# Kernel optimization log

Hardware: AMD Instinct MI355X
Metric: run time of the kernel (lower is better)

Reference implementation:

```python
import jax, jax.numpy as jnp
import numpy as np

L = 4        # n_layers
C = 512      # channels = d_model
NH = 16      # n_heads
DH = 32      # d_head (hard-coded in source)
DFF = 4 * C  # FeedForward hidden size
B, HH, WW = 4, 32, 32
GN_GROUPS, GN_EPS, LN_EPS = 16, 1e-6, 1e-5


def setup_inputs() -> dict:
    key = jax.random.key(0)
    ks = jax.random.split(key, 32)
    w = lambda k, s: (jax.random.normal(k, s, jnp.float32) * 0.02)
    return {
        "x": jax.random.normal(ks[0], (B, C, HH, WW), jnp.float32),
        # GroupNorm affine
        "gn_w": jnp.ones((C,), jnp.float32),
        "gn_b": jnp.zeros((C,), jnp.float32),
        # 1x1 conv in/out, stored as [C_in, C_out]
        "pin_w": w(ks[1], (C, C)), "pin_b": jnp.zeros((C,), jnp.float32),
        "pout_w": w(ks[2], (C, C)), "pout_b": jnp.zeros((C,), jnp.float32),
        # per-layer stacked params
        "ln1_w": jnp.ones((L, C), jnp.float32), "ln1_b": jnp.zeros((L, C), jnp.float32),
        "wq": w(ks[3], (L, C, C)), "wk": w(ks[4], (L, C, C)), "wv": w(ks[5], (L, C, C)),
        "wo": w(ks[6], (L, C, C)), "bo": jnp.zeros((L, C), jnp.float32),
        "ln3_w": jnp.ones((L, C), jnp.float32), "ln3_b": jnp.zeros((L, C), jnp.float32),
        "ff1_w": w(ks[7], (L, C, 2 * DFF)), "ff1_b": jnp.zeros((L, 2 * DFF), jnp.float32),
        "ff2_w": w(ks[8], (L, DFF, C)), "ff2_b": jnp.zeros((L, C), jnp.float32),
    }


def _group_norm(x, w, b):
    bsz, c, h, ww = x.shape
    xg = x.reshape(bsz, GN_GROUPS, c // GN_GROUPS, h, ww)
    m = xg.mean(axis=(2, 3, 4), keepdims=True)
    v = xg.var(axis=(2, 3, 4), keepdims=True)
    xn = ((xg - m) * jax.lax.rsqrt(v + GN_EPS)).reshape(bsz, c, h, ww)
    return xn * w[None, :, None, None] + b[None, :, None, None]


def _layer_norm(x, w, b):
    m = x.mean(axis=-1, keepdims=True)
    v = x.var(axis=-1, keepdims=True)
    return (x - m) * jax.lax.rsqrt(v + LN_EPS) * w + b


def reference(x, gn_w, gn_b, pin_w, pin_b, pout_w, pout_b,
              ln1_w, ln1_b, wq, wk, wv, wo, bo,
              ln3_w, ln3_b, ff1_w, ff1_b, ff2_w, ff2_b):
    b, c, h, w_ = x.shape
    x_in = x
    x = _group_norm(x, gn_w, gn_b)
    x = jnp.einsum('bchw,co->bohw', x, pin_w) + pin_b[None, :, None, None]
    x = x.transpose(0, 2, 3, 1).reshape(b, h * w_, c)  # [b, n, c]
    n = h * w_
    nh = c // DH
    scale = DH ** -0.5
    for l in range(L):
        hx = _layer_norm(x, ln1_w[l], ln1_b[l])
        q = (hx @ wq[l]).reshape(b, n, nh, DH)
        k = (hx @ wk[l]).reshape(b, n, nh, DH)
        v = (hx @ wv[l]).reshape(b, n, nh, DH)
        attn = jax.nn.softmax(jnp.einsum('bihd,bjhd->bhij', q, k) * scale, axis=-1)
        o = jnp.einsum('bhij,bjhd->bihd', attn, v).reshape(b, n, c)
        x = o @ wo[l] + bo[l] + x
        hx = _layer_norm(x, ln3_w[l], ln3_b[l])
        p = hx @ ff1_w[l] + ff1_b[l]
        a, g = jnp.split(p, 2, axis=-1)
        x = (a * jax.nn.gelu(g, approximate=False)) @ ff2_w[l] + ff2_b[l] + x
    x = x.reshape(b, h, w_, c).transpose(0, 3, 1, 2)
    x = jnp.einsum('bchw,co->bohw', x, pout_w) + pout_b[None, :, None, None]
    return x + x_in
```

## Files before the change

### kernel.cpp

```cpp
#include <hip/hip_runtime.h>
#include <math.h>


typedef __bf16 bf16x8_t __attribute__((ext_vector_type(8)));
typedef float f32x4 __attribute__((ext_vector_type(4)));

__device__ __forceinline__ unsigned short f2bf(float f) {
  unsigned u = __float_as_uint(f);
  return (unsigned short)((u + 0x7FFFu + ((u >> 16) & 1u)) >> 16);
}
__device__ __forceinline__ float gelu_exact(float x) {
  return 0.5f * x * (1.f + erff(x * 0.70710678118654752440f));
}

__global__ __launch_bounds__(256) void gn_kernel(
    const float* __restrict__ X, const float* __restrict__ w,
    const float* __restrict__ b, float* __restrict__ Y) {
  int blk = blockIdx.x;
  int g = blk & 15;
  const float* xp = X + (size_t)blk * 32 * 1024;
  float* yp = Y + (size_t)blk * 32 * 1024;
  int tid = threadIdx.x;
  float sum = 0.f, sq = 0.f;
  const float4* x4 = (const float4*)xp;
  for (int i = tid; i < 8192; i += 256) {
    float4 v = x4[i];
    sum += v.x + v.y + v.z + v.w;
    sq += v.x * v.x + v.y * v.y + v.z * v.z + v.w * v.w;
  }
  #pragma unroll
  for (int off = 32; off; off >>= 1) {
    sum += __shfl_xor(sum, off);
    sq += __shfl_xor(sq, off);
  }
  __shared__ float s0[4], s1[4];
  int wid = tid >> 6, lane = tid & 63;
  if (lane == 0) { s0[wid] = sum; s1[wid] = sq; }
  __syncthreads();
  sum = s0[0] + s0[1] + s0[2] + s0[3];
  sq = s1[0] + s1[1] + s1[2] + s1[3];
  float mean = sum * (1.f / 32768.f);
  float var = sq * (1.f / 32768.f) - mean * mean;
  float rstd = rsqrtf(var + 1e-6f);
  float4* y4 = (float4*)yp;
  for (int i = tid; i < 8192; i += 256) {
    int ch = g * 32 + (i >> 8);
    float sc = rstd * w[ch];
    float sh = b[ch] - mean * sc;
    float4 v = x4[i];
    float4 o;
    o.x = v.x * sc + sh; o.y = v.y * sc + sh;
    o.z = v.z * sc + sh; o.w = v.w * sc + sh;
    y4[i] = o;
  }
}

__global__ __launch_bounds__(256) void ln_kernel(
    const float* __restrict__ X, const float* __restrict__ w,
    const float* __restrict__ b, unsigned short* __restrict__ Y) {
  int row = blockIdx.x * 4 + (threadIdx.x >> 6);
  int lane = threadIdx.x & 63;
  const float4* xr = (const float4*)(X + (size_t)row * 512);
  float4 v0 = xr[lane];
  float4 v1 = xr[lane + 64];
  float sum = v0.x + v0.y + v0.z + v0.w + v1.x + v1.y + v1.z + v1.w;
  float sq = v0.x * v0.x + v0.y * v0.y + v0.z * v0.z + v0.w * v0.w +
             v1.x * v1.x + v1.y * v1.y + v1.z * v1.z + v1.w * v1.w;
  #pragma unroll
  for (int off = 32; off; off >>= 1) {
    sum += __shfl_xor(sum, off);
    sq += __shfl_xor(sq, off);
  }
  float mean = sum * (1.f / 512.f);
  float var = sq * (1.f / 512.f) - mean * mean;
  float rstd = rsqrtf(var + 1e-5f);
  unsigned short* yr = Y + (size_t)row * 512;
  int c0 = lane * 4, c1 = lane * 4 + 256;
  const float4 w0 = *(const float4*)&w[c0], b0v = *(const float4*)&b[c0];
  const float4 w1 = *(const float4*)&w[c1], b1v = *(const float4*)&b[c1];
  unsigned p0 = (unsigned)f2bf((v0.x - mean) * rstd * w0.x + b0v.x) |
                ((unsigned)f2bf((v0.y - mean) * rstd * w0.y + b0v.y) << 16);
  unsigned p1 = (unsigned)f2bf((v0.z - mean) * rstd * w0.z + b0v.z) |
                ((unsigned)f2bf((v0.w - mean) * rstd * w0.w + b0v.w) << 16);
  unsigned p2 = (unsigned)f2bf((v1.x - mean) * rstd * w1.x + b1v.x) |
                ((unsigned)f2bf((v1.y - mean) * rstd * w1.y + b1v.y) << 16);
  unsigned p3 = (unsigned)f2bf((v1.z - mean) * rstd * w1.z + b1v.z) |
                ((unsigned)f2bf((v1.w - mean) * rstd * w1.w + b1v.w) << 16);
  uint2 q0 = {p0, p1}, q1 = {p2, p3};
  *(uint2*)&yr[c0] = q0;
  *(uint2*)&yr[c1] = q1;
}

__global__ void wtc_kernel(const float* __restrict__ in,
                           unsigned short* __restrict__ out, int rows,
                           int cols, float scale) {
  __shared__ float t[32][33];
  int z = blockIdx.z;
  const float* ip = in + (size_t)z * rows * cols;
  unsigned short* op = out + (size_t)z * rows * cols;
  int r0 = blockIdx.y * 32, c0 = blockIdx.x * 32;
  for (int rr = threadIdx.y; rr < 32; rr += 8)
    t[rr][threadIdx.x] = ip[(size_t)(r0 + rr) * cols + c0 + threadIdx.x];
  __syncthreads();
  for (int rr = threadIdx.y; rr < 32; rr += 8)
    op[(size_t)(c0 + rr) * rows + r0 + threadIdx.x] =
        f2bf(t[threadIdx.x][rr] * scale);
}

template <int TM, int TN, int MODE>
__global__ __launch_bounds__(256) void mgemm(
    const short* __restrict__ A, int lda, const short* __restrict__ B0,
    const short* __restrict__ B1, const short* __restrict__ B2, float* C0,
    float* C1, float* C2, unsigned short* Cb, int ldc,
    const float* __restrict__ bias, const float* resid, int K, int ggoff) {
  constexpr int WM = TM / 2, WN = TN / 2, MF = WM / 16, NF = WN / 16;
  constexpr int ASL = TM / 32;
  constexpr int BSL = TN / 32;
  __shared__ short As[2][TM][64];
  __shared__ short Bs[2][TN][64];
  __shared__ short Bs2[MODE == 2 ? 2 : 1][MODE == 2 ? TN : 1][64];

  const short* B = B0;
  float* C = C0;
  if (blockIdx.z == 1) { B = B1; C = C1; }
  else if (blockIdx.z == 2) { B = B2; C = C2; }
  const short* Bg = (MODE == 2) ? B0 + (size_t)ggoff * K : nullptr;

  int tid = threadIdx.x;
  int bm = blockIdx.y * TM, bn = blockIdx.x * TN;

  f32x4 acc[MF][NF];
  f32x4 acc2[MODE == 2 ? MF : 1][MODE == 2 ? NF : 1];
  #pragma unroll
  for (int m = 0; m < MF; ++m)
    #pragma unroll
    for (int n = 0; n < NF; ++n) {
      acc[m][n] = (f32x4)0.f;
      if (MODE == 2) acc2[m][n] = (f32x4)0.f;
    }

  int wid = tid >> 6, lane = tid & 63;
  int wr = wid >> 1, wc = wid & 1;
  int lrow = lane & 15, lhk = lane >> 4;

  bf16x8_t ra[ASL], rb[BSL], rb2[MODE == 2 ? BSL : 1];

  auto load_regs = [&](int k0) {
    #pragma unroll
    for (int i = 0; i < ASL; ++i) {
      int slot = tid + i * 256, r = slot >> 3, s = slot & 7;
      ra[i] = *(const bf16x8_t*)(A + (size_t)(bm + r) * lda + k0 + s * 8);
    }
    #pragma unroll
    for (int i = 0; i < BSL; ++i) {
      int slot = tid + i * 256, r = slot >> 3, s = slot & 7;
      rb[i] = *(const bf16x8_t*)(B + (size_t)(bn + r) * K + k0 + s * 8);
      if (MODE == 2)
        rb2[i] = *(const bf16x8_t*)(Bg + (size_t)(bn + r) * K + k0 + s * 8);
    }
  };
  auto store_lds = [&](int bufi) {
    #pragma unroll
    for (int i = 0; i < ASL; ++i) {
      int slot = tid + i * 256, r = slot >> 3, s = slot & 7;
      *(bf16x8_t*)&As[bufi][r][(s ^ (r & 7)) * 8] = ra[i];
    }
    #pragma unroll
    for (int i = 0; i < BSL; ++i) {
      int slot = tid + i * 256, r = slot >> 3, s = slot & 7;
      *(bf16x8_t*)&Bs[bufi][r][(s ^ (r & 7)) * 8] = rb[i];
      if (MODE == 2) *(bf16x8_t*)&Bs2[bufi][r][(s ^ (r & 7)) * 8] = rb2[i];
    }
  };
  auto compute = [&](int bufi) {
    bf16x8_t af[2][MF], bfr[2][NF], bf2[MODE == 2 ? 2 : 1][MODE == 2 ? NF : 1];
    #pragma unroll
    for (int ks = 0; ks < 2; ++ks) {
      int sl = ks * 4 + lhk;
      int ph = (sl ^ (lrow & 7)) * 8;
      #pragma unroll
      for (int m = 0; m < MF; ++m)
        af[ks][m] = *(const bf16x8_t*)&As[bufi][wr * WM + m * 16 + lrow][ph];
      #pragma unroll
      for (int n = 0; n < NF; ++n) {
        bfr[ks][n] = *(const bf16x8_t*)&Bs[bufi][wc * WN + n * 16 + lrow][ph];
        if (MODE == 2)
          bf2[ks][n] = *(const bf16x8_t*)&Bs2[bufi][wc * WN + n * 16 + lrow][ph];
      }
    }
    #pragma unroll
    for (int ks = 0; ks < 2; ++ks)
      #pragma unroll
      for (int m = 0; m < MF; ++m)
        #pragma unroll
        for (int n = 0; n < NF; ++n) {
          acc[m][n] = __builtin_amdgcn_mfma_f32_16x16x32_bf16(
              af[ks][m], bfr[ks][n], acc[m][n], 0, 0, 0);
          if (MODE == 2)
            acc2[m][n] = __builtin_amdgcn_mfma_f32_16x16x32_bf16(
                af[ks][m], bf2[ks][n], acc2[m][n], 0, 0, 0);
        }
  };

  int ns = K >> 6;
  load_regs(0);
  store_lds(0);
  __syncthreads();
  int buf = 0;
  for (int t = 0; t < ns; ++t) {
    bool more = (t + 1 < ns);
    if (more) load_regs((t + 1) << 6);
    compute(buf);
    if (more) store_lds(buf ^ 1);
    __syncthreads();
    buf ^= 1;
  }

  int row0 = bm + wr * WM + lhk * 4;
  int col0 = bn + wc * WN + lrow;
  #pragma unroll
  for (int m = 0; m < MF; ++m) {
    #pragma unroll
    for (int n = 0; n < NF; ++n) {
      int col = col0 + n * 16;
      if (MODE == 0) {
        float bv = bias ? bias[col] : 0.f;
        #pragma unroll
        for (int j = 0; j < 4; ++j) {
          int row = row0 + m * 16 + j;
          C[(size_t)row * ldc + col] = acc[m][n][j] + bv;
        }
      } else if (MODE == 1) {
        float bv = bias[col];
        #pragma unroll
        for (int j = 0; j < 4; ++j) {
          int row = row0 + m * 16 + j;
          float v = acc[m][n][j] + bv + resid[(size_t)row * ldc + col];
          C[(size_t)row * ldc + col] = v;
          Cb[(size_t)row * ldc + col] = f2bf(v);
        }
      } else if (MODE == 2) {
        float ba = bias[col], bg = bias[ggoff + col];
        #pragma unroll
        for (int j = 0; j < 4; ++j) {
          int row = row0 + m * 16 + j;
          float a = acc[m][n][j] + ba;
          float g = acc2[m][n][j] + bg;
          Cb[(size_t)row * ldc + col] = f2bf(a * gelu_exact(g));
        }
      } else {
        unsigned short* Co = (unsigned short*)C;
        #pragma unroll
        for (int j = 0; j < 4; ++j) {
          int row = row0 + m * 16 + j;
          Co[(size_t)row * ldc + col] = f2bf(acc[m][n][j]);
        }
      }
    }
  }
}

__global__ __launch_bounds__(256) void fattn_kernel(
    const unsigned short* __restrict__ Q, const unsigned short* __restrict__ K,
    const unsigned short* __restrict__ V, unsigned short* __restrict__ O) {
  constexpr int QT = 128, KT = 64;
  __shared__ __bf16 Ks[KT][40];
  __shared__ __bf16 Vs[32][68];
  __shared__ __bf16 Ps[4][32][68];

  int h = blockIdx.y, bb = blockIdx.z;
  int q0 = blockIdx.x * QT;
  int tid = threadIdx.x;
  int wid = tid >> 6, lane = tid & 63;
  int lrow = lane & 15, lhk = lane >> 4;

  const unsigned short* Qb = Q + (size_t)bb * 1024 * 512 + h * 32;
  const unsigned short* Kb = K + (size_t)bb * 1024 * 512 + h * 32;
  const unsigned short* Vb = V + (size_t)bb * 1024 * 512 + h * 32;

  bf16x8_t qa[2];
  #pragma unroll
  for (int m = 0; m < 2; ++m)
    qa[m] = *(const bf16x8_t*)(
        Qb + (size_t)(q0 + wid * 32 + m * 16 + lrow) * 512 + lhk * 8);

  int kr = tid >> 2, kp = tid & 3;
  int vk = tid & 63, vd0 = (tid >> 6) * 8;

  bf16x8_t kreg, vreg;
  auto gload = [&](int kt) {
    kreg = *(const bf16x8_t*)(Kb + (size_t)(kt + kr) * 512 + kp * 8);
    vreg = *(const bf16x8_t*)(Vb + (size_t)(kt + vk) * 512 + vd0);
  };
  auto sstore = [&]() {
    *(bf16x8_t*)&Ks[kr][kp * 8] = kreg;
    #pragma unroll
    for (int i = 0; i < 8; ++i) Vs[vd0 + i][vk] = vreg[i];
  };

  f32x4 o[2][2];
  float lpart[2][4];
  #pragma unroll
  for (int m = 0; m < 2; ++m) {
    o[m][0] = (f32x4)0.f; o[m][1] = (f32x4)0.f;
    #pragma unroll
    for (int j = 0; j < 4; ++j) lpart[m][j] = 0.f;
  }

  gload(0);
  for (int t = 0; t < 16; ++t) {
    sstore();
    __syncthreads();
    if (t < 15) gload((t + 1) * KT);

    bf16x8_t kb[4];
    #pragma unroll
    for (int n = 0; n < 4; ++n)
      kb[n] = *(const bf16x8_t*)&Ks[n * 16 + lrow][lhk * 8];
    f32x4 s[2][4];
    #pragma unroll
    for (int m = 0; m < 2; ++m)
      #pragma unroll
      for (int n = 0; n < 4; ++n)
        s[m][n] = __builtin_amdgcn_mfma_f32_16x16x32_bf16(qa[m], kb[n],
                                                          (f32x4)0.f, 0, 0, 0);

    #pragma unroll
    for (int m = 0; m < 2; ++m)
      #pragma unroll
      for (int j = 0; j < 4; ++j) {
        float p0 = __expf(s[m][0][j]), p1 = __expf(s[m][1][j]);
        float p2 = __expf(s[m][2][j]), p3 = __expf(s[m][3][j]);
        lpart[m][j] += (p0 + p1) + (p2 + p3);
        int prow = m * 16 + lhk * 4 + j;
        Ps[wid][prow][lrow] = (__bf16)p0;
        Ps[wid][prow][16 + lrow] = (__bf16)p1;
        Ps[wid][prow][32 + lrow] = (__bf16)p2;
        Ps[wid][prow][48 + lrow] = (__bf16)p3;
      }

    #pragma unroll
    for (int ks = 0; ks < 2; ++ks) {
      bf16x8_t pa[2], vbf[2];
      #pragma unroll
      for (int m = 0; m < 2; ++m)
        pa[m] = *(const bf16x8_t*)&Ps[wid][m * 16 + lrow][ks * 32 + lhk * 8];
      #pragma unroll
      for (int dn = 0; dn < 2; ++dn)
        vbf[dn] = *(const bf16x8_t*)&Vs[dn * 16 + lrow][ks * 32 + lhk * 8];
      #pragma unroll
      for (int m = 0; m < 2; ++m)
        #pragma unroll
        for (int dn = 0; dn < 2; ++dn)
          o[m][dn] = __builtin_amdgcn_mfma_f32_16x16x32_bf16(pa[m], vbf[dn],
                                                             o[m][dn], 0, 0, 0);
    }
    __syncthreads();
  }

  #pragma unroll
  for (int m = 0; m < 2; ++m)
    #pragma unroll
    for (int j = 0; j < 4; ++j) {
      float l = lpart[m][j];
      #pragma unroll
      for (int off = 1; off < 16; off <<= 1) l += __shfl_xor(l, off);
      float inv = 1.f / l;
      int row = q0 + wid * 32 + m * 16 + lhk * 4 + j;
      #pragma unroll
      for (int dn = 0; dn < 2; ++dn)
        O[(size_t)(bb * 1024 + row) * 512 + h * 32 + dn * 16 + lrow] =
            __builtin_bit_cast(unsigned short, (__bf16)(o[m][dn][j] * inv));
    }
}

__global__ void out_kernel(const float* __restrict__ y,
                           const float* __restrict__ pb,
                           const float* __restrict__ xin,
                           float* __restrict__ out) {
  __shared__ float t[32][33];
  int b = blockIdx.z;
  int o0 = blockIdx.x * 32, n0 = blockIdx.y * 32;
  const float* yp = y + (size_t)b * 1024 * 512;
  for (int rr = threadIdx.y; rr < 32; rr += 8)
    t[rr][threadIdx.x] = yp[(size_t)(n0 + rr) * 512 + o0 + threadIdx.x];
  __syncthreads();
  for (int rr = threadIdx.y; rr < 32; rr += 8) {
    int o = o0 + rr;
    size_t idx = ((size_t)b * 512 + o) * 1024 + n0 + threadIdx.x;
    out[idx] = t[threadIdx.x][rr] + pb[o] + xin[idx];
  }
}

extern "C" void kernel_launch(void* const* d_in, const int* in_sizes, int n_in,
                              void* d_out, int out_size, void* d_ws,
                              size_t ws_size, hipStream_t stream) {
  const float* x_in = (const float*)d_in[0];
  const float* gn_w = (const float*)d_in[1];
  const float* gn_b = (const float*)d_in[2];
  const float* pin_w = (const float*)d_in[3];
  const float* pin_b = (const float*)d_in[4];
  const float* pout_w = (const float*)d_in[5];
  const float* pout_b = (const float*)d_in[6];
  const float* ln1_w = (const float*)d_in[7];
  const float* ln1_b = (const float*)d_in[8];
  const float* wq = (const float*)d_in[9];
  const float* wk = (const float*)d_in[10];
  const float* wv = (const float*)d_in[11];
  const float* wo = (const float*)d_in[12];
  const float* bo = (const float*)d_in[13];
  const float* ln3_w = (const float*)d_in[14];
  const float* ln3_b = (const float*)d_in[15];
  const float* ff1_w = (const float*)d_in[16];
  const float* ff1_b = (const float*)d_in[17];
  const float* ff2_w = (const float*)d_in[18];
  const float* ff2_b = (const float*)d_in[19];

  char* wsb = (char*)d_ws;
  float* XTOK = (float*)wsb;
  char* R = wsb + (8u << 20);
  unsigned short* Qbf = (unsigned short*)R;
  unsigned short* Kbf = (unsigned short*)(R + (4u << 20));
  unsigned short* Vbf = (unsigned short*)(R + (8u << 20));
  unsigned short* G2b = (unsigned short*)R;
  float* XTy = (float*)(R + (16u << 20));
  float* GNt = (float*)R;
  unsigned short* XTb = (unsigned short*)(wsb + (32u << 20));
  unsigned short* HXb = (unsigned short*)(wsb + (36u << 20));
  unsigned short* Obf = (unsigned short*)(wsb + (40u << 20));
  unsigned short* XTOKb = (unsigned short*)(wsb + (44u << 20));
  unsigned short* W = (unsigned short*)(wsb + (48u << 20));
  const size_t S = 262144;
  unsigned short* pinT = W;
  unsigned short* poutT = W + S;
  unsigned short* wqT = W + 2 * S;
  unsigned short* wkT = wqT + 4 * S;
  unsigned short* wvT = wkT + 4 * S;
  unsigned short* woT = wvT + 4 * S;
  unsigned short* ff1T = woT + 4 * S;
  unsigned short* ff2T = ff1T + 4 * (512 * 4096);

  dim3 tb32(32, 8);
  const float qscale = 0.17677669529663687f;

  wtc_kernel<<<dim3(16, 16, 1), tb32, 0, stream>>>(pin_w, pinT, 512, 512, 1.f);
  wtc_kernel<<<dim3(16, 16, 1), tb32, 0, stream>>>(pout_w, poutT, 512, 512, 1.f);
  wtc_kernel<<<dim3(16, 16, 4), tb32, 0, stream>>>(wq, wqT, 512, 512, qscale);
  wtc_kernel<<<dim3(16, 16, 4), tb32, 0, stream>>>(wk, wkT, 512, 512, 1.f);
  wtc_kernel<<<dim3(16, 16, 4), tb32, 0, stream>>>(wv, wvT, 512, 512, 1.f);
  wtc_kernel<<<dim3(16, 16, 4), tb32, 0, stream>>>(wo, woT, 512, 512, 1.f);
  wtc_kernel<<<dim3(128, 16, 4), tb32, 0, stream>>>(ff1_w, ff1T, 512, 4096, 1.f);
  wtc_kernel<<<dim3(16, 64, 4), tb32, 0, stream>>>(ff2_w, ff2T, 2048, 512, 1.f);

  gn_kernel<<<64, 256, 0, stream>>>(x_in, gn_w, gn_b, GNt);
  wtc_kernel<<<dim3(32, 16, 4), tb32, 0, stream>>>(GNt, XTb, 512, 1024, 1.f);
  mgemm<128, 64, 0><<<dim3(8, 32, 1), 256, 0, stream>>>(
      (const short*)XTb, 512, (const short*)pinT, nullptr, nullptr, XTOK,
      nullptr, nullptr, nullptr, 512, pin_b, nullptr, 512, 0);

  for (int l = 0; l < 4; ++l) {
    const short* wqT_l = (const short*)(wqT + (size_t)l * S);
    const short* wkT_l = (const short*)(wkT + (size_t)l * S);
    const short* wvT_l = (const short*)(wvT + (size_t)l * S);
    const short* woT_l = (const short*)(woT + (size_t)l * S);
    const short* ff1T_l = (const short*)(ff1T + (size_t)l * 512 * 4096);
    const short* ff2T_l = (const short*)(ff2T + (size_t)l * 2048 * 512);

    ln_kernel<<<1024, 256, 0, stream>>>(XTOK, ln1_w + l * 512, ln1_b + l * 512,
                                        HXb);
    mgemm<128, 64, 3><<<dim3(8, 32, 3), 256, 0, stream>>>(
        (const short*)HXb, 512, wqT_l, wkT_l, wvT_l, (float*)Qbf, (float*)Kbf,
        (float*)Vbf, nullptr, 512, nullptr, nullptr, 512, 0);
    fattn_kernel<<<dim3(8, 16, 4), 256, 0, stream>>>(Qbf, Kbf, Vbf, Obf);
    mgemm<128, 64, 1><<<dim3(8, 32, 1), 256, 0, stream>>>(
        (const short*)Obf, 512, woT_l, nullptr, nullptr, XTOK, nullptr,
        nullptr, XTOKb, 512, bo + l * 512, XTOK, 512, 0);
    ln_kernel<<<1024, 256, 0, stream>>>(XTOK, ln3_w + l * 512, ln3_b + l * 512,
                                        HXb);
    mgemm<128, 64, 2><<<dim3(32, 32, 1), 256, 0, stream>>>(
        (const short*)HXb, 512, ff1T_l, nullptr, nullptr, nullptr, nullptr,
        nullptr, G2b, 2048, ff1_b + l * 4096, nullptr, 512, 2048);
    mgemm<128, 64, 1><<<dim3(8, 32, 1), 256, 0, stream>>>(
        (const short*)G2b, 2048, ff2T_l, nullptr, nullptr, XTOK, nullptr,
        nullptr, XTOKb, 512, ff2_b + l * 512, XTOK, 2048, 0);
  }
  mgemm<128, 64, 0><<<dim3(8, 32, 1), 256, 0, stream>>>(
      (const short*)XTOKb, 512, (const short*)poutT, nullptr, nullptr, XTy,
      nullptr, nullptr, nullptr, 512, nullptr, nullptr, 512, 0);
  out_kernel<<<dim3(16, 32, 4), tb32, 0, stream>>>(XTy, pout_b, x_in,
                                                   (float*)d_out);
}
```

Baseline: 580.1 us.

## Batch weight conversions into one launch, fuse GN apply and output epilogue, XCD-aware tile mapping

Replaces the nine separate weight transpose/convert launches with one table-driven conversion kernel. The GroupNorm apply step moves into the input transpose through per-channel scale/shift values, so the normalized fp32 intermediate is never written out. The final out-projection GEMM gets a new epilogue that writes NCHW output with bias and residual directly, which removes out_kernel and its scratch buffer. GEMM block indices are remapped so that each XCD takes a contiguous band of M rows for better L2 locality, at the cost of extra index arithmetic.

```diff
diff --git a/kernel.cpp b/kernel.cpp
--- a/kernel.cpp
+++ b/kernel.cpp
@@ -13,16 +13,15 @@
   return 0.5f * x * (1.f + erff(x * 0.70710678118654752440f));
 }
 
-__global__ __launch_bounds__(256) void gn_kernel(
+__global__ __launch_bounds__(256) void gn_stats(
     const float* __restrict__ X, const float* __restrict__ w,
-    const float* __restrict__ b, float* __restrict__ Y) {
+    const float* __restrict__ b, float* __restrict__ sc,
+    float* __restrict__ sh) {
   int blk = blockIdx.x;
-  int g = blk & 15;
-  const float* xp = X + (size_t)blk * 32 * 1024;
-  float* yp = Y + (size_t)blk * 32 * 1024;
+  int g = blk & 15, bb = blk >> 4;
+  const float4* x4 = (const float4*)(X + (size_t)blk * 32768);
   int tid = threadIdx.x;
   float sum = 0.f, sq = 0.f;
-  const float4* x4 = (const float4*)xp;
   for (int i = tid; i < 8192; i += 256) {
     float4 v = x4[i];
     sum += v.x + v.y + v.z + v.w;
@@ -42,17 +41,47 @@
   float mean = sum * (1.f / 32768.f);
   float var = sq * (1.f / 32768.f) - mean * mean;
   float rstd = rsqrtf(var + 1e-6f);
-  float4* y4 = (float4*)yp;
-  for (int i = tid; i < 8192; i += 256) {
-    int ch = g * 32 + (i >> 8);
-    float sc = rstd * w[ch];
-    float sh = b[ch] - mean * sc;
-    float4 v = x4[i];
-    float4 o;
-    o.x = v.x * sc + sh; o.y = v.y * sc + sh;
-    o.z = v.z * sc + sh; o.w = v.w * sc + sh;
-    y4[i] = o;
-  }
+  if (tid < 32) {
+    int ch = g * 32 + tid;
+    float s_ = rstd * w[ch];
+    sc[bb * 512 + ch] = s_;
+    sh[bb * 512 + ch] = b[ch] - mean * s_;
+  }
+}
+
+struct CvtEnt {
+  const float* src; unsigned short* dst;
+  const float* rs; const float* rsh;
+  int rows, cols, nmat, pre; float scale;
+};
+struct CvtTab { CvtEnt e[9]; };
+
+__global__ __launch_bounds__(256) void cvt_all(CvtTab tab) {
+  __shared__ float t[32][33];
+  int blk = blockIdx.x;
+  int ei = 0;
+  #pragma unroll
+  for (int i = 1; i < 9; ++i)
+    if (blk >= tab.e[i].pre) ei = i;
+  const CvtEnt E = tab.e[ei];
+  int local = blk - E.pre;
+  int tcx = E.cols >> 5;
+  int tpm = tcx * (E.rows >> 5);
+  int mat = local / tpm, tt = local - mat * tpm;
+  int r0 = (tt / tcx) << 5, c0 = (tt - (tt / tcx) * tcx) << 5;
+  const float* sp = E.src + (size_t)mat * E.rows * E.cols;
+  unsigned short* dp = E.dst + (size_t)mat * E.rows * E.cols;
+  const float* rsp = E.rs ? E.rs + (size_t)mat * E.rows : nullptr;
+  const float* rshp = E.rsh ? E.rsh + (size_t)mat * E.rows : nullptr;
+  int tx = threadIdx.x;
+  for (int rr = threadIdx.y; rr < 32; rr += 8) {
+    float s_ = rsp ? rsp[r0 + rr] : E.scale;
+    float h_ = rshp ? rshp[r0 + rr] : 0.f;
+    t[rr][tx] = sp[(size_t)(r0 + rr) * E.cols + c0 + tx] * s_ + h_;
+  }
+  __syncthreads();
+  for (int rr = threadIdx.y; rr < 32; rr += 8)
+    dp[(size_t)(c0 + rr) * E.rows + r0 + tx] = f2bf(t[tx][rr]);
 }
 
 __global__ __launch_bounds__(256) void ln_kernel(
@@ -91,22 +120,6 @@
   *(uint2*)&yr[c1] = q1;
 }
 
-__global__ void wtc_kernel(const float* __restrict__ in,
-                           unsigned short* __restrict__ out, int rows,
-                           int cols, float scale) {
-  __shared__ float t[32][33];
-  int z = blockIdx.z;
-  const float* ip = in + (size_t)z * rows * cols;
-  unsigned short* op = out + (size_t)z * rows * cols;
-  int r0 = blockIdx.y * 32, c0 = blockIdx.x * 32;
-  for (int rr = threadIdx.y; rr < 32; rr += 8)
-    t[rr][threadIdx.x] = ip[(size_t)(r0 + rr) * cols + c0 + threadIdx.x];
-  __syncthreads();
-  for (int rr = threadIdx.y; rr < 32; rr += 8)
-    op[(size_t)(c0 + rr) * rows + r0 + threadIdx.x] =
-        f2bf(t[threadIdx.x][rr] * scale);
-}
-
 template <int TM, int TN, int MODE>
 __global__ __launch_bounds__(256) void mgemm(
     const short* __restrict__ A, int lda, const short* __restrict__ B0,
@@ -120,14 +133,25 @@
   __shared__ short Bs[2][TN][64];
   __shared__ short Bs2[MODE == 2 ? 2 : 1][MODE == 2 ? TN : 1][64];
 
+  int flat = (blockIdx.z * gridDim.y + blockIdx.y) * gridDim.x + blockIdx.x;
+  int xcd = flat & 7;
+  int pos = flat >> 3;
+  int gz = gridDim.z;
+  int zz = pos % gz;
+  pos /= gz;
+  int bandH = gridDim.y >> 3;
+  int m_loc = pos % bandH;
+  int bn_i = pos / bandH;
+  int bm = (xcd * bandH + m_loc) * TM;
+  int bn = bn_i * TN;
+
   const short* B = B0;
   float* C = C0;
-  if (blockIdx.z == 1) { B = B1; C = C1; }
-  else if (blockIdx.z == 2) { B = B2; C = C2; }
+  if (zz == 1) { B = B1; C = C1; }
+  else if (zz == 2) { B = B2; C = C2; }
   const short* Bg = (MODE == 2) ? B0 + (size_t)ggoff * K : nullptr;
 
   int tid = threadIdx.x;
-  int bm = blockIdx.y * TM, bn = blockIdx.x * TN;
 
   f32x4 acc[MF][NF];
   f32x4 acc2[MODE == 2 ? MF : 1][MODE == 2 ? NF : 1];
@@ -248,13 +272,22 @@
           float g = acc2[m][n][j] + bg;
           Cb[(size_t)row * ldc + col] = f2bf(a * gelu_exact(g));
         }
-      } else {
+      } else if (MODE == 3) {
         unsigned short* Co = (unsigned short*)C;
         #pragma unroll
         for (int j = 0; j < 4; ++j) {
           int row = row0 + m * 16 + j;
           Co[(size_t)row * ldc + col] = f2bf(acc[m][n][j]);
         }
+      } else {
+        float bv = bias[col];
+        int row = row0 + m * 16;
+        int b_ = row >> 10, n0 = row & 1023;
+        size_t oidx = ((size_t)b_ * 512 + col) * 1024 + n0;
+        float4 xi = *(const float4*)&resid[oidx];
+        float4 ov = {acc[m][n][0] + bv + xi.x, acc[m][n][1] + bv + xi.y,
+                     acc[m][n][2] + bv + xi.z, acc[m][n][3] + bv + xi.w};
+        *(float4*)&C[oidx] = ov;
       }
     }
   }
@@ -372,24 +405,6 @@
         O[(size_t)(bb * 1024 + row) * 512 + h * 32 + dn * 16 + lrow] =
             __builtin_bit_cast(unsigned short, (__bf16)(o[m][dn][j] * inv));
     }
-}
-
-__global__ void out_kernel(const float* __restrict__ y,
-                           const float* __restrict__ pb,
-                           const float* __restrict__ xin,
-                           float* __restrict__ out) {
-  __shared__ float t[32][33];
-  int b = blockIdx.z;
-  int o0 = blockIdx.x * 32, n0 = blockIdx.y * 32;
-  const float* yp = y + (size_t)b * 1024 * 512;
-  for (int rr = threadIdx.y; rr < 32; rr += 8)
-    t[rr][threadIdx.x] = yp[(size_t)(n0 + rr) * 512 + o0 + threadIdx.x];
-  __syncthreads();
-  for (int rr = threadIdx.y; rr < 32; rr += 8) {
-    int o = o0 + rr;
-    size_t idx = ((size_t)b * 512 + o) * 1024 + n0 + threadIdx.x;
-    out[idx] = t[threadIdx.x][rr] + pb[o] + xin[idx];
-  }
 }
 
 extern "C" void kernel_launch(void* const* d_in, const int* in_sizes, int n_in,
@@ -423,8 +438,8 @@
   unsigned short* Kbf = (unsigned short*)(R + (4u << 20));
   unsigned short* Vbf = (unsigned short*)(R + (8u << 20));
   unsigned short* G2b = (unsigned short*)R;
-  float* XTy = (float*)(R + (16u << 20));
-  float* GNt = (float*)R;
+  float* gnsc = (float*)(R + (16u << 20));
+  float* gnsh = gnsc + 2048;
   unsigned short* XTb = (unsigned short*)(wsb + (32u << 20));
   unsigned short* HXb = (unsigned short*)(wsb + (36u << 20));
   unsigned short* Obf = (unsigned short*)(wsb + (40u << 20));
@@ -440,20 +455,29 @@
   unsigned short* ff1T = woT + 4 * S;
   unsigned short* ff2T = ff1T + 4 * (512 * 4096);
 
-  dim3 tb32(32, 8);
   const float qscale = 0.17677669529663687f;
 
-  wtc_kernel<<<dim3(16, 16, 1), tb32, 0, stream>>>(pin_w, pinT, 512, 512, 1.f);
-  wtc_kernel<<<dim3(16, 16, 1), tb32, 0, stream>>>(pout_w, poutT, 512, 512, 1.f);
-  wtc_kernel<<<dim3(16, 16, 4), tb32, 0, stream>>>(wq, wqT, 512, 512, qscale);
-  wtc_kernel<<<dim3(16, 16, 4), tb32, 0, stream>>>(wk, wkT, 512, 512, 1.f);
-  wtc_kernel<<<dim3(16, 16, 4), tb32, 0, stream>>>(wv, wvT, 512, 512, 1.f);
-  wtc_kernel<<<dim3(16, 16, 4), tb32, 0, stream>>>(wo, woT, 512, 512, 1.f);
-  wtc_kernel<<<dim3(128, 16, 4), tb32, 0, stream>>>(ff1_w, ff1T, 512, 4096, 1.f);
-  wtc_kernel<<<dim3(16, 64, 4), tb32, 0, stream>>>(ff2_w, ff2T, 2048, 512, 1.f);
-
-  gn_kernel<<<64, 256, 0, stream>>>(x_in, gn_w, gn_b, GNt);
-  wtc_kernel<<<dim3(32, 16, 4), tb32, 0, stream>>>(GNt, XTb, 512, 1024, 1.f);
+  gn_stats<<<64, 256, 0, stream>>>(x_in, gn_w, gn_b, gnsc, gnsh);
+
+  CvtTab tab;
+  int pre = 0;
+  auto add = [&](int i, const float* src, unsigned short* dst, int rows,
+                 int cols, int nmat, float sc, const float* rs,
+                 const float* rsh) {
+    tab.e[i] = {src, dst, rs, rsh, rows, cols, nmat, pre, sc};
+    pre += nmat * (rows / 32) * (cols / 32);
+  };
+  add(0, x_in, XTb, 512, 1024, 4, 1.f, gnsc, gnsh);
+  add(1, pin_w, pinT, 512, 512, 1, 1.f, nullptr, nullptr);
+  add(2, pout_w, poutT, 512, 512, 1, 1.f, nullptr, nullptr);
+  add(3, wq, wqT, 512, 512, 4, qscale, nullptr, nullptr);
+  add(4, wk, wkT, 512, 512, 4, 1.f, nullptr, nullptr);
+  add(5, wv, wvT, 512, 512, 4, 1.f, nullptr, nullptr);
+  add(6, wo, woT, 512, 512, 4, 1.f, nullptr, nullptr);
+  add(7, ff1_w, ff1T, 512, 4096, 4, 1.f, nullptr, nullptr);
+  add(8, ff2_w, ff2T, 2048, 512, 4, 1.f, nullptr, nullptr);
+  cvt_all<<<pre, dim3(32, 8), 0, stream>>>(tab);
+
   mgemm<128, 64, 0><<<dim3(8, 32, 1), 256, 0, stream>>>(
       (const short*)XTb, 512, (const short*)pinT, nullptr, nullptr, XTOK,
       nullptr, nullptr, nullptr, 512, pin_b, nullptr, 512, 0);
@@ -484,9 +508,7 @@
         (const short*)G2b, 2048, ff2T_l, nullptr, nullptr, XTOK, nullptr,
         nullptr, XTOKb, 512, ff2_b + l * 512, XTOK, 2048, 0);
   }
-  mgemm<128, 64, 0><<<dim3(8, 32, 1), 256, 0, stream>>>(
-      (const short*)XTOKb, 512, (const short*)poutT, nullptr, nullptr, XTy,
-      nullptr, nullptr, nullptr, 512, nullptr, nullptr, 512, 0);
-  out_kernel<<<dim3(16, 32, 4), tb32, 0, stream>>>(XTy, pout_b, x_in,
-                                                   (float*)d_out);
-}
+  mgemm<128, 64, 4><<<dim3(8, 32, 1), 256, 0, stream>>>(
+      (const short*)XTOKb, 512, (const short*)poutT, nullptr, nullptr,
+      (float*)d_out, nullptr, nullptr, nullptr, 512, pout_b, x_in, 512, 0);
+}
```

After: 549.7 us. 1.06x faster.
